# Optimization experiments

Hardware: AMD Instinct MI355X
Metric: run time of the kernel (lower is better)

## Reference

```python
import jax, jax.numpy as jnp
import numpy as np

N = 100000   # nodes
E = 500000   # edges
DN = 64      # node feat dim
DE = 64      # edge feat dim
D = 128      # hidden = in_feats = out_feats
TD = 64      # time-encoding dim


def setup_inputs() -> dict:
    key = jax.random.key(0)
    ks = jax.random.split(key, 20)
    s = 0.05
    inp = {
        'nfeat': jax.random.normal(ks[0], (N, DN), dtype=jnp.float32),
        'efeat': jax.random.normal(ks[1], (E, DE), dtype=jnp.float32),
        'src': jax.random.randint(ks[2], (E,), 0, N),
        'dst': jax.random.randint(ks[3], (E,), 0, N),
        'ts': jax.random.uniform(ks[4], (E,), dtype=jnp.float32) * 1000.0,
    }
    i = 5
    for l in (1, 2):
        inp[f'W_self{l}'] = jax.random.normal(ks[i], (D + TD, D), dtype=jnp.float32) * s; i += 1
        inp[f'b_self{l}'] = jnp.zeros((D,), dtype=jnp.float32)
        inp[f'W_neigh{l}'] = jax.random.normal(ks[i], (D, D), dtype=jnp.float32) * s; i += 1
        inp[f'b_neigh{l}'] = jnp.zeros((D,), dtype=jnp.float32)
        inp[f'omega{l}'] = jax.random.normal(ks[i], (TD,), dtype=jnp.float32); i += 1
        inp[f'phase{l}'] = jax.random.normal(ks[i], (TD,), dtype=jnp.float32); i += 1
    return inp


def _tsage_layer(src_prev, dst_prev, src, dst, ts, W_self, b_self, W_neigh, b_neigh, omega, phase):
    # cosine time encoding per edge: [E, TD]
    te = jnp.cos(ts[:, None] * omega[None, :] + phase[None, :])
    # temporal-neighborhood mean: per node, mean of features of incident edges
    sum_n = (jax.ops.segment_sum(dst_prev, src, num_segments=N)
             + jax.ops.segment_sum(src_prev, dst, num_segments=N))      # [N, D]
    ones = jnp.ones((src.shape[0], 1), dtype=src_prev.dtype)
    cnt = (jax.ops.segment_sum(ones, src, num_segments=N)
           + jax.ops.segment_sum(ones, dst, num_segments=N))            # [N, 1]
    mean_n = sum_n / jnp.maximum(cnt, 1.0)                              # [N, D]
    neigh_proj = mean_n @ W_neigh + b_neigh                             # project once per node
    src_out = jnp.concatenate([src_prev, te], axis=1) @ W_self + b_self + neigh_proj[src]
    dst_out = jnp.concatenate([dst_prev, te], axis=1) @ W_self + b_self + neigh_proj[dst]
    # dropout in eval mode (identity), then activation (relu)
    return jax.nn.relu(src_out), jax.nn.relu(dst_out)


def reference(nfeat, efeat, src, dst, ts,
              W_self1, b_self1, W_neigh1, b_neigh1, omega1, phase1,
              W_self2, b_self2, W_neigh2, b_neigh2, omega2, phase2):
    # combine_feats: per-edge gather-concat of endpoint node feats with edge feats
    src_feat = jnp.concatenate([nfeat[src], efeat], axis=1)  # [E, D]
    dst_feat = jnp.concatenate([nfeat[dst], efeat], axis=1)  # [E, D]
    params = [
        (W_self1, b_self1, W_neigh1, b_neigh1, omega1, phase1),
        (W_self2, b_self2, W_neigh2, b_neigh2, omega2, phase2),
    ]
    for p in params:
        src_feat, dst_feat = _tsage_layer(src_feat, dst_feat, src, dst, ts, *p)
    return src_feat, dst_feat
```

## Files before the change

kernel.cpp:

```cpp
#include <hip/hip_runtime.h>
#include <cstdint>
#include <cmath>

#define NN 100000
#define EE 500000
#define CAP 64

typedef __attribute__((ext_vector_type(8))) short short8v;
typedef __attribute__((ext_vector_type(4))) float f32x4;

static __device__ __forceinline__ unsigned short f2bf_rne(float x) {
    unsigned u = __float_as_uint(x);
    u += 0x7FFFu + ((u >> 16) & 1u);
    return (unsigned short)(u >> 16);
}

static __device__ __forceinline__ void split8(float4 a, float4 b,
                                              short8v* hi, short8v* lo) {
    union { short8v v; unsigned u[4]; } H, L;
    float f[8] = {a.x, a.y, a.z, a.w, b.x, b.y, b.z, b.w};
#pragma unroll
    for (int p = 0; p < 4; ++p) {
        unsigned u0 = __float_as_uint(f[2 * p]);
        unsigned u1 = __float_as_uint(f[2 * p + 1]);
        H.u[p] = (u0 >> 16) | (u1 & 0xFFFF0000u);
        float r0 = f[2 * p]     - __uint_as_float(u0 & 0xFFFF0000u);
        float r1 = f[2 * p + 1] - __uint_as_float(u1 & 0xFFFF0000u);
        L.u[p] = (unsigned)f2bf_rne(r0) | ((unsigned)f2bf_rne(r1) << 16);
    }
    *hi = H.v; *lo = L.v;
}

__global__ __launch_bounds__(256) void k_build(const int* __restrict__ src,
                                               const int* __restrict__ dst,
                                               int* __restrict__ pos,
                                               int* __restrict__ eidx) {
    int e = blockIdx.x * 256 + threadIdx.x;
    if (e >= EE) return;
    int s = src[e], d = dst[e];
    int sl = atomicAdd(&pos[s], 1);
    if (sl < CAP) eidx[(size_t)s * CAP + sl] = (e << 1) | 1;
    int dl = atomicAdd(&pos[d], 1);
    if (dl < CAP) eidx[(size_t)d * CAP + dl] = (e << 1);
}

__global__ __launch_bounds__(256) void k_wt(const float* __restrict__ W, int K,
                                            unsigned short* __restrict__ H,
                                            unsigned short* __restrict__ L) {
    int idx = blockIdx.x * 256 + threadIdx.x;
    if (idx >= K * 128) return;
    int k = idx >> 7, c = idx & 127;
    float x = W[idx];
    unsigned u = __float_as_uint(x);
    H[(size_t)c * K + k] = (unsigned short)(u >> 16);
    float r = x - __uint_as_float(u & 0xFFFF0000u);
    L[(size_t)c * K + k] = f2bf_rne(r);
}

template <int LAYER>
__global__ __launch_bounds__(256) void k_agg(const float* __restrict__ featS,
                                             const float* __restrict__ featD,
                                             const float* __restrict__ nfeat,
                                             const float* __restrict__ efeat,
                                             const int* __restrict__ src,
                                             const int* __restrict__ dst,
                                             const int* __restrict__ pos,
                                             const int* __restrict__ eidx,
                                             float* __restrict__ mean) {
    int w = (blockIdx.x * 256 + threadIdx.x) >> 6;
    int lane = threadIdx.x & 63;
    if (w >= NN) return;
    int half = lane >> 5, cl = lane & 31;
    int d = pos[w];
    int dd = min(d, CAP);
    const int* lst = eidx + (size_t)w * CAP;
    float ax = 0.f, ay = 0.f, az = 0.f, aw = 0.f;
    for (int j = half; j < dd; j += 2) {
        int entry = lst[j];
        int e = entry >> 1, side = entry & 1;
        const float* p;
        if (LAYER == 1) {
            if (cl < 16) {
                int other = side ? dst[e] : src[e];
                p = nfeat + (size_t)other * 64 + cl * 4;
            } else {
                p = efeat + (size_t)e * 64 + (cl - 16) * 4;
            }
        } else {
            p = (side ? featD : featS) + (size_t)e * 128 + cl * 4;
        }
        float4 v = *(const float4*)p;
        ax += v.x; ay += v.y; az += v.z; aw += v.w;
    }
    ax += __shfl_xor(ax, 32); ay += __shfl_xor(ay, 32);
    az += __shfl_xor(az, 32); aw += __shfl_xor(aw, 32);
    if (half == 0) {
        float inv = 1.0f / fmaxf((float)d, 1.0f);
        float4 r; r.x = ax * inv; r.y = ay * inv; r.z = az * inv; r.w = aw * inv;
        *(float4*)(mean + (size_t)w * 128 + cl * 4) = r;
    }
}

__global__ __launch_bounds__(256, 3) void k_neigh_mfma(
        const float* __restrict__ mean,
        const unsigned short* __restrict__ WtH,
        const unsigned short* __restrict__ WtL,
        const float* __restrict__ bias,
        float* __restrict__ outp) {
    const int tid  = threadIdx.x;
    const int n0   = blockIdx.x * 128;
    const int lane = tid & 63;
    const int w    = tid >> 6;
    const int krow = lane & 15;
    const int kgrp = lane >> 4;

    const float* rb[2];
#pragma unroll
    for (int rt = 0; rt < 2; ++rt) {
        int n = min(n0 + w * 32 + rt * 16 + krow, NN - 1);
        rb[rt] = mean + (size_t)n * 128;
    }

    f32x4 acc[2][8] = {};
#pragma unroll
    for (int ch = 0; ch < 4; ++ch) {
        const int koff = ch * 32 + kgrp * 8;
        short8v Ah[2], Al[2];
#pragma unroll
        for (int rt = 0; rt < 2; ++rt) {
            float4 x0 = *(const float4*)(rb[rt] + koff);
            float4 x1 = *(const float4*)(rb[rt] + koff + 4);
            split8(x0, x1, &Ah[rt], &Al[rt]);
        }
#pragma unroll
        for (int ct = 0; ct < 8; ++ct) {
            int c = ct * 16 + krow;
            short8v Bh = *(const short8v*)(WtH + (size_t)c * 128 + koff);
            short8v Bl = *(const short8v*)(WtL + (size_t)c * 128 + koff);
#pragma unroll
            for (int rt = 0; rt < 2; ++rt) {
                acc[rt][ct] = __builtin_amdgcn_mfma_f32_16x16x32_bf16(Ah[rt], Bh, acc[rt][ct], 0, 0, 0);
                acc[rt][ct] = __builtin_amdgcn_mfma_f32_16x16x32_bf16(Ah[rt], Bl, acc[rt][ct], 0, 0, 0);
                acc[rt][ct] = __builtin_amdgcn_mfma_f32_16x16x32_bf16(Al[rt], Bh, acc[rt][ct], 0, 0, 0);
            }
        }
    }

    float bcol[8];
#pragma unroll
    for (int ct = 0; ct < 8; ++ct) bcol[ct] = bias[ct * 16 + krow];
#pragma unroll
    for (int rt = 0; rt < 2; ++rt) {
#pragma unroll
        for (int j = 0; j < 4; ++j) {
            int n = n0 + w * 32 + rt * 16 + kgrp * 4 + j;
            if (n < NN) {
                float* op = outp + (size_t)n * 128;
#pragma unroll
                for (int ct = 0; ct < 8; ++ct)
                    op[ct * 16 + krow] = acc[rt][ct][j] + bcol[ct];
            }
        }
    }
}

template <int LAYER>
__global__ __launch_bounds__(256, 3) void k_edge_mfma(
        const float* __restrict__ featS, const float* __restrict__ featD,
        const float* __restrict__ nfeat, const float* __restrict__ efeat,
        float* __restrict__ outS, float* __restrict__ outD,
        const int* __restrict__ src, const int* __restrict__ dst,
        const float* __restrict__ ts,
        const unsigned short* __restrict__ WtH,
        const unsigned short* __restrict__ WtL,
        const float* __restrict__ bias,
        const float* __restrict__ neigh,
        const float* __restrict__ omega, const float* __restrict__ phase) {
    __shared__ unsigned short teH[64][72];
    __shared__ unsigned short teL[64][72];

    const int tid  = threadIdx.x;
    const int e0   = blockIdx.x * 64;
    const int lane = tid & 63;
    const int w    = tid >> 6;
    const int krow = lane & 15;
    const int kgrp = lane >> 4;

    {
        const int tl = tid & 63;
        const int j0 = (tid >> 6) * 16;
        const float tval = ts[min(e0 + tl, EE - 1)];
#pragma unroll
        for (int j = 0; j < 16; j += 2) {
            int jj = j0 + j;
            float c0 = cosf(fmaf(tval, omega[jj],     phase[jj]));
            float c1 = cosf(fmaf(tval, omega[jj + 1], phase[jj + 1]));
            unsigned u0 = __float_as_uint(c0), u1 = __float_as_uint(c1);
            *(unsigned*)&teH[tl][jj] = (u0 >> 16) | (u1 & 0xFFFF0000u);
            float r0 = c0 - __uint_as_float(u0 & 0xFFFF0000u);
            float r1 = c1 - __uint_as_float(u1 & 0xFFFF0000u);
            *(unsigned*)&teL[tl][jj] =
                (unsigned)f2bf_rne(r0) | ((unsigned)f2bf_rne(r1) << 16);
        }
    }
    __syncthreads();

    const float* rbN[2];
    const float* rbE[2];
#pragma unroll
    for (int rt = 0; rt < 2; ++rt) {
        int row = w * 32 + rt * 16 + krow;
        int e = min(e0 + (row & 63), EE - 1);
        if (LAYER == 1) {
            int node = (row < 64) ? src[e] : dst[e];
            rbN[rt] = nfeat + (size_t)node * 64;
            rbE[rt] = efeat + (size_t)e * 64;
        } else {
            rbN[rt] = ((row < 64) ? featS : featD) + (size_t)e * 128;
            rbE[rt] = nullptr;
        }
    }

    f32x4 acc[2][8] = {};

#pragma unroll
    for (int ch = 0; ch < 4; ++ch) {
        const int koff = ch * 32 + kgrp * 8;
        short8v Ah[2], Al[2];
#pragma unroll
        for (int rt = 0; rt < 2; ++rt) {
            const float* p;
            if (LAYER == 1) {
                p = (ch < 2) ? (rbN[rt] + koff) : (rbE[rt] + (koff - 64));
            } else {
                p = rbN[rt] + koff;
            }
            float4 x0 = *(const float4*)p;
            float4 x1 = *(const float4*)(p + 4);
            split8(x0, x1, &Ah[rt], &Al[rt]);
        }
#pragma unroll
        for (int ct = 0; ct < 8; ++ct) {
            int c = ct * 16 + krow;
            short8v Bh = *(const short8v*)(WtH + (size_t)c * 192 + koff);
            short8v Bl = *(const short8v*)(WtL + (size_t)c * 192 + koff);
#pragma unroll
            for (int rt = 0; rt < 2; ++rt) {
                acc[rt][ct] = __builtin_amdgcn_mfma_f32_16x16x32_bf16(Ah[rt], Bh, acc[rt][ct], 0, 0, 0);
                acc[rt][ct] = __builtin_amdgcn_mfma_f32_16x16x32_bf16(Ah[rt], Bl, acc[rt][ct], 0, 0, 0);
                acc[rt][ct] = __builtin_amdgcn_mfma_f32_16x16x32_bf16(Al[rt], Bh, acc[rt][ct], 0, 0, 0);
            }
        }
    }

#pragma unroll
    for (int ch = 4; ch < 6; ++ch) {
        const int koff = ch * 32 + kgrp * 8;
        const int kt = koff - 128;
        short8v Ah[2], Al[2];
#pragma unroll
        for (int rt = 0; rt < 2; ++rt) {
            int el = (w * 32 + rt * 16 + krow) & 63;
            Ah[rt] = *(const short8v*)&teH[el][kt];
            Al[rt] = *(const short8v*)&teL[el][kt];
        }
#pragma unroll
        for (int ct = 0; ct < 8; ++ct) {
            int c = ct * 16 + krow;
            short8v Bh = *(const short8v*)(WtH + (size_t)c * 192 + koff);
            short8v Bl = *(const short8v*)(WtL + (size_t)c * 192 + koff);
#pragma unroll
            for (int rt = 0; rt < 2; ++rt) {
                acc[rt][ct] = __builtin_amdgcn_mfma_f32_16x16x32_bf16(Ah[rt], Bh, acc[rt][ct], 0, 0, 0);
                acc[rt][ct] = __builtin_amdgcn_mfma_f32_16x16x32_bf16(Ah[rt], Bl, acc[rt][ct], 0, 0, 0);
                acc[rt][ct] = __builtin_amdgcn_mfma_f32_16x16x32_bf16(Al[rt], Bh, acc[rt][ct], 0, 0, 0);
            }
        }
    }

    float bcol[8];
#pragma unroll
    for (int ct = 0; ct < 8; ++ct) bcol[ct] = bias[ct * 16 + krow];
#pragma unroll
    for (int rt = 0; rt < 2; ++rt) {
#pragma unroll
        for (int j = 0; j < 4; ++j) {
            int row = w * 32 + rt * 16 + kgrp * 4 + j;
            int e = e0 + (row & 63);
            if (e < EE) {
                bool isS = row < 64;
                int node = isS ? src[e] : dst[e];
                const float* np = neigh + (size_t)node * 128;
                float* op = (isS ? outS : outD) + (size_t)e * 128;
#pragma unroll
                for (int ct = 0; ct < 8; ++ct) {
                    float v2 = acc[rt][ct][j] + bcol[ct] + np[ct * 16 + krow];
                    op[ct * 16 + krow] = fmaxf(v2, 0.f);
                }
            }
        }
    }
}

extern "C" void kernel_launch(void* const* d_in, const int* in_sizes, int n_in,
                              void* d_out, int out_size, void* d_ws, size_t ws_size,
                              hipStream_t stream) {
    const float* nfeat = (const float*)d_in[0];
    const float* efeat = (const float*)d_in[1];
    const int*   src   = (const int*)d_in[2];
    const int*   dst   = (const int*)d_in[3];
    const float* ts    = (const float*)d_in[4];
    const float* Wself[2]  = {(const float*)d_in[5],  (const float*)d_in[11]};
    const float* bself[2]  = {(const float*)d_in[6],  (const float*)d_in[12]};
    const float* Wneigh[2] = {(const float*)d_in[7],  (const float*)d_in[13]};
    const float* bneigh[2] = {(const float*)d_in[8],  (const float*)d_in[14]};
    const float* omega[2]  = {(const float*)d_in[9],  (const float*)d_in[15]};
    const float* phase[2]  = {(const float*)d_in[10], (const float*)d_in[16]};

    float* outS = (float*)d_out;
    float* outD = outS + (size_t)EE * 128;

    float* mean  = (float*)d_ws;
    float* neigh = mean + (size_t)NN * 128;
    int*   pos   = (int*)(neigh + (size_t)NN * 128);
    int*   eidx  = pos + NN;
    unsigned short* wb = (unsigned short*)(eidx + (size_t)NN * CAP);
    unsigned short* WsH[2] = {wb,                 wb + 2 * 128 * 192};
    unsigned short* WsL[2] = {wb + 128 * 192,     wb + 3 * 128 * 192};
    unsigned short* wn = wb + 4 * 128 * 192;
    unsigned short* WnH[2] = {wn,                 wn + 2 * 128 * 128};
    unsigned short* WnL[2] = {wn + 128 * 128,     wn + 3 * 128 * 128};

    hipMemsetAsync(pos, 0, NN * sizeof(int), stream);
    k_build<<<(EE + 255) / 256, 256, 0, stream>>>(src, dst, pos, eidx);
    for (int l = 0; l < 2; ++l) {
        k_wt<<<(192 * 128 + 255) / 256, 256, 0, stream>>>(Wself[l], 192, WsH[l], WsL[l]);
        k_wt<<<(128 * 128 + 255) / 256, 256, 0, stream>>>(Wneigh[l], 128, WnH[l], WnL[l]);
    }

    k_agg<1><<<(NN * 64 + 255) / 256, 256, 0, stream>>>(outS, outD, nfeat, efeat,
                                                        src, dst, pos, eidx, mean);
    k_neigh_mfma<<<(NN + 127) / 128, 256, 0, stream>>>(mean, WnH[0], WnL[0], bneigh[0], neigh);
    k_edge_mfma<1><<<(EE + 63) / 64, 256, 0, stream>>>(outS, outD, nfeat, efeat,
                                                       outS, outD, src, dst, ts,
                                                       WsH[0], WsL[0], bself[0], neigh,
                                                       omega[0], phase[0]);

    k_agg<2><<<(NN * 64 + 255) / 256, 256, 0, stream>>>(outS, outD, nfeat, efeat,
                                                        src, dst, pos, eidx, mean);
    k_neigh_mfma<<<(NN + 127) / 128, 256, 0, stream>>>(mean, WnH[1], WnL[1], bneigh[1], neigh);
    k_edge_mfma<2><<<(EE + 63) / 64, 256, 0, stream>>>(outS, outD, nfeat, efeat,
                                                       outS, outD, src, dst, ts,
                                                       WsH[1], WsL[1], bself[1], neigh,
                                                       omega[1], phase[1]);
}
```

Baseline: 2.121 ms.

## Stage edge-GEMM A tiles via LDS DMA, 2x2 warp tiling, denser adjacency

The edge GEMM now streams the gathered A rows into a double-buffered, swizzled LDS tile using global_load_lds DMA. Warps are retiled 2x2 so each wave reuses 4 A row tiles against 4 weight column tiles, which cuts redundant weight loads. The adjacency list now stores the neighbor node id next to the edge id, sparing an extra src/dst lookup in aggregation, and aggregation uses wider per-lane loads with 4 edges in flight. CAP drops from 64 to 48, which silently truncates the neighbor sum for any node with degree above 48, a risk for correctness. The occupancy hints are removed.

```diff
diff --git a/kernel.cpp b/kernel.cpp
--- a/kernel.cpp
+++ b/kernel.cpp
@@ -4,7 +4,7 @@
 
 #define NN 100000
 #define EE 500000
-#define CAP 64
+#define CAP 48
 
 typedef __attribute__((ext_vector_type(8))) short short8v;
 typedef __attribute__((ext_vector_type(4))) float f32x4;
@@ -31,17 +31,23 @@
     *hi = H.v; *lo = L.v;
 }
 
+static __device__ __forceinline__ void lds_dma16(const void* g, void* l) {
+    __builtin_amdgcn_global_load_lds(
+        (const __attribute__((address_space(1))) unsigned int*)g,
+        (__attribute__((address_space(3))) unsigned int*)l, 16, 0, 0);
+}
+
 __global__ __launch_bounds__(256) void k_build(const int* __restrict__ src,
                                                const int* __restrict__ dst,
                                                int* __restrict__ pos,
-                                               int* __restrict__ eidx) {
+                                               int2* __restrict__ inc) {
     int e = blockIdx.x * 256 + threadIdx.x;
     if (e >= EE) return;
     int s = src[e], d = dst[e];
     int sl = atomicAdd(&pos[s], 1);
-    if (sl < CAP) eidx[(size_t)s * CAP + sl] = (e << 1) | 1;
+    if (sl < CAP) inc[(size_t)s * CAP + sl] = make_int2((e << 1) | 1, d);
     int dl = atomicAdd(&pos[d], 1);
-    if (dl < CAP) eidx[(size_t)d * CAP + dl] = (e << 1);
+    if (dl < CAP) inc[(size_t)d * CAP + dl] = make_int2((e << 1), s);
 }
 
 __global__ __launch_bounds__(256) void k_wt(const float* __restrict__ W, int K,
@@ -62,46 +68,51 @@
                                              const float* __restrict__ featD,
                                              const float* __restrict__ nfeat,
                                              const float* __restrict__ efeat,
-                                             const int* __restrict__ src,
-                                             const int* __restrict__ dst,
                                              const int* __restrict__ pos,
-                                             const int* __restrict__ eidx,
+                                             const int2* __restrict__ inc,
                                              float* __restrict__ mean) {
     int w = (blockIdx.x * 256 + threadIdx.x) >> 6;
     int lane = threadIdx.x & 63;
     if (w >= NN) return;
-    int half = lane >> 5, cl = lane & 31;
+    int q = lane >> 4, cl = lane & 15;
     int d = pos[w];
     int dd = min(d, CAP);
-    const int* lst = eidx + (size_t)w * CAP;
-    float ax = 0.f, ay = 0.f, az = 0.f, aw = 0.f;
-    for (int j = half; j < dd; j += 2) {
-        int entry = lst[j];
-        int e = entry >> 1, side = entry & 1;
+    const int2* lst = inc + (size_t)w * CAP;
+    float a0 = 0.f, a1 = 0.f, a2 = 0.f, a3 = 0.f;
+    float a4 = 0.f, a5 = 0.f, a6 = 0.f, a7 = 0.f;
+    for (int j = q; j < dd; j += 4) {
+        int2 en = lst[j];
+        int e = en.x >> 1, side = en.x & 1;
         const float* p;
         if (LAYER == 1) {
-            if (cl < 16) {
-                int other = side ? dst[e] : src[e];
-                p = nfeat + (size_t)other * 64 + cl * 4;
-            } else {
-                p = efeat + (size_t)e * 64 + (cl - 16) * 4;
-            }
+            p = (cl < 8) ? (nfeat + (size_t)en.y * 64 + cl * 8)
+                         : (efeat + (size_t)e * 64 + (cl - 8) * 8);
         } else {
-            p = (side ? featD : featS) + (size_t)e * 128 + cl * 4;
-        }
-        float4 v = *(const float4*)p;
-        ax += v.x; ay += v.y; az += v.z; aw += v.w;
-    }
-    ax += __shfl_xor(ax, 32); ay += __shfl_xor(ay, 32);
-    az += __shfl_xor(az, 32); aw += __shfl_xor(aw, 32);
-    if (half == 0) {
+            p = (side ? featD : featS) + (size_t)e * 128 + cl * 8;
+        }
+        float4 v0 = *(const float4*)p;
+        float4 v1 = *(const float4*)(p + 4);
+        a0 += v0.x; a1 += v0.y; a2 += v0.z; a3 += v0.w;
+        a4 += v1.x; a5 += v1.y; a6 += v1.z; a7 += v1.w;
+    }
+#pragma unroll
+    for (int m = 16; m <= 32; m <<= 1) {
+        a0 += __shfl_xor(a0, m); a1 += __shfl_xor(a1, m);
+        a2 += __shfl_xor(a2, m); a3 += __shfl_xor(a3, m);
+        a4 += __shfl_xor(a4, m); a5 += __shfl_xor(a5, m);
+        a6 += __shfl_xor(a6, m); a7 += __shfl_xor(a7, m);
+    }
+    if (q == 0) {
         float inv = 1.0f / fmaxf((float)d, 1.0f);
-        float4 r; r.x = ax * inv; r.y = ay * inv; r.z = az * inv; r.w = aw * inv;
-        *(float4*)(mean + (size_t)w * 128 + cl * 4) = r;
-    }
-}
-
-__global__ __launch_bounds__(256, 3) void k_neigh_mfma(
+        float4 r0, r1;
+        r0.x = a0 * inv; r0.y = a1 * inv; r0.z = a2 * inv; r0.w = a3 * inv;
+        r1.x = a4 * inv; r1.y = a5 * inv; r1.z = a6 * inv; r1.w = a7 * inv;
+        *(float4*)(mean + (size_t)w * 128 + cl * 8) = r0;
+        *(float4*)(mean + (size_t)w * 128 + cl * 8 + 4) = r1;
+    }
+}
+
+__global__ __launch_bounds__(256) void k_neigh_mfma(
         const float* __restrict__ mean,
         const unsigned short* __restrict__ WtH,
         const unsigned short* __restrict__ WtL,
@@ -111,61 +122,64 @@
     const int n0   = blockIdx.x * 128;
     const int lane = tid & 63;
     const int w    = tid >> 6;
+    const int wr   = w >> 1, wc = w & 1;
     const int krow = lane & 15;
     const int kgrp = lane >> 4;
 
-    const float* rb[2];
-#pragma unroll
-    for (int rt = 0; rt < 2; ++rt) {
-        int n = min(n0 + w * 32 + rt * 16 + krow, NN - 1);
+    const float* rb[4];
+#pragma unroll
+    for (int rt = 0; rt < 4; ++rt) {
+        int n = min(n0 + wr * 64 + rt * 16 + krow, NN - 1);
         rb[rt] = mean + (size_t)n * 128;
     }
 
-    f32x4 acc[2][8] = {};
+    f32x4 acc[4][4] = {};
 #pragma unroll
     for (int ch = 0; ch < 4; ++ch) {
         const int koff = ch * 32 + kgrp * 8;
-        short8v Ah[2], Al[2];
-#pragma unroll
-        for (int rt = 0; rt < 2; ++rt) {
+        short8v Ah[4], Al[4];
+#pragma unroll
+        for (int rt = 0; rt < 4; ++rt) {
             float4 x0 = *(const float4*)(rb[rt] + koff);
             float4 x1 = *(const float4*)(rb[rt] + koff + 4);
             split8(x0, x1, &Ah[rt], &Al[rt]);
         }
-#pragma unroll
-        for (int ct = 0; ct < 8; ++ct) {
-            int c = ct * 16 + krow;
-            short8v Bh = *(const short8v*)(WtH + (size_t)c * 128 + koff);
-            short8v Bl = *(const short8v*)(WtL + (size_t)c * 128 + koff);
-#pragma unroll
-            for (int rt = 0; rt < 2; ++rt) {
-                acc[rt][ct] = __builtin_amdgcn_mfma_f32_16x16x32_bf16(Ah[rt], Bh, acc[rt][ct], 0, 0, 0);
-                acc[rt][ct] = __builtin_amdgcn_mfma_f32_16x16x32_bf16(Ah[rt], Bl, acc[rt][ct], 0, 0, 0);
-                acc[rt][ct] = __builtin_amdgcn_mfma_f32_16x16x32_bf16(Al[rt], Bh, acc[rt][ct], 0, 0, 0);
-            }
-        }
-    }
-
-    float bcol[8];
-#pragma unroll
-    for (int ct = 0; ct < 8; ++ct) bcol[ct] = bias[ct * 16 + krow];
-#pragma unroll
-    for (int rt = 0; rt < 2; ++rt) {
+        short8v Bh[4], Bl[4];
+#pragma unroll
+        for (int ct = 0; ct < 4; ++ct) {
+            int c = wc * 64 + ct * 16 + krow;
+            Bh[ct] = *(const short8v*)(WtH + (size_t)c * 128 + koff);
+            Bl[ct] = *(const short8v*)(WtL + (size_t)c * 128 + koff);
+        }
+#pragma unroll
+        for (int ct = 0; ct < 4; ++ct)
+#pragma unroll
+            for (int rt = 0; rt < 4; ++rt) {
+                acc[rt][ct] = __builtin_amdgcn_mfma_f32_16x16x32_bf16(Ah[rt], Bh[ct], acc[rt][ct], 0, 0, 0);
+                acc[rt][ct] = __builtin_amdgcn_mfma_f32_16x16x32_bf16(Ah[rt], Bl[ct], acc[rt][ct], 0, 0, 0);
+                acc[rt][ct] = __builtin_amdgcn_mfma_f32_16x16x32_bf16(Al[rt], Bh[ct], acc[rt][ct], 0, 0, 0);
+            }
+    }
+
+    float bcol[4];
+#pragma unroll
+    for (int ct = 0; ct < 4; ++ct) bcol[ct] = bias[wc * 64 + ct * 16 + krow];
+#pragma unroll
+    for (int rt = 0; rt < 4; ++rt)
 #pragma unroll
         for (int j = 0; j < 4; ++j) {
-            int n = n0 + w * 32 + rt * 16 + kgrp * 4 + j;
+            int n = n0 + wr * 64 + rt * 16 + kgrp * 4 + j;
             if (n < NN) {
                 float* op = outp + (size_t)n * 128;
 #pragma unroll
-                for (int ct = 0; ct < 8; ++ct)
-                    op[ct * 16 + krow] = acc[rt][ct][j] + bcol[ct];
-            }
-        }
-    }
+                for (int ct = 0; ct < 4; ++ct)
+                    op[wc * 64 + ct * 16 + krow] = acc[rt][ct][j] + bcol[ct];
+            }
+        }
 }
 
 template <int LAYER>
-__global__ __launch_bounds__(256, 3) void k_edge_mfma(
+__global__ __launch_bounds__(256) void k_edge_mfma(
         const float* __restrict__ featS, const float* __restrict__ featD,
         const float* __restrict__ nfeat, const float* __restrict__ efeat,
         float* __restrict__ outS, float* __restrict__ outD,
@@ -176,6 +190,7 @@
         const float* __restrict__ bias,
         const float* __restrict__ neigh,
         const float* __restrict__ omega, const float* __restrict__ phase) {
+    __shared__ float Abuf[2][128][32];
     __shared__ unsigned short teH[64][72];
     __shared__ unsigned short teL[64][72];
 
@@ -183,6 +198,7 @@
     const int e0   = blockIdx.x * 64;
     const int lane = tid & 63;
     const int w    = tid >> 6;
+    const int wr   = w >> 1, wc = w & 1;
     const int krow = lane & 15;
     const int kgrp = lane >> 4;
 
@@ -203,89 +219,108 @@
                 (unsigned)f2bf_rne(r0) | ((unsigned)f2bf_rne(r1) << 16);
         }
     }
-    __syncthreads();
-
-    const float* rbN[2];
-    const float* rbE[2];
-#pragma unroll
-    for (int rt = 0; rt < 2; ++rt) {
-        int row = w * 32 + rt * 16 + krow;
+
+    const float* gbN[4];
+    const float* gbE[4];
+#pragma unroll
+    for (int qq = 0; qq < 4; ++qq) {
+        int row = w * 32 + qq * 8 + (lane >> 3);
         int e = min(e0 + (row & 63), EE - 1);
         if (LAYER == 1) {
             int node = (row < 64) ? src[e] : dst[e];
-            rbN[rt] = nfeat + (size_t)node * 64;
-            rbE[rt] = efeat + (size_t)e * 64;
+            gbN[qq] = nfeat + (size_t)node * 64;
+            gbE[qq] = efeat + (size_t)e * 64;
         } else {
-            rbN[rt] = ((row < 64) ? featS : featD) + (size_t)e * 128;
-            rbE[rt] = nullptr;
-        }
-    }
-
-    f32x4 acc[2][8] = {};
+            gbN[qq] = ((row < 64) ? featS : featD) + (size_t)e * 128;
+            gbE[qq] = nullptr;
+        }
+    }
+    const int pslot = lane & 7;
+
+    auto dma_chunk = [&](int b, int ch) {
+#pragma unroll
+        for (int qq = 0; qq < 4; ++qq) {
+            int row = w * 32 + qq * 8 + (lane >> 3);
+            int pg = (pslot - row) & 7;
+            const float* gsrc;
+            if (LAYER == 1)
+                gsrc = ((ch < 2) ? (gbN[qq] + ch * 32) : (gbE[qq] + (ch - 2) * 32)) + pg * 4;
+            else
+                gsrc = gbN[qq] + ch * 32 + pg * 4;
+            lds_dma16(gsrc, &Abuf[b][(w * 4 + qq) * 8][0]);
+        }
+    };
+
+    f32x4 acc[4][4] = {};
+    dma_chunk(0, 0);
 
 #pragma unroll
     for (int ch = 0; ch < 4; ++ch) {
+        __syncthreads();
+        if (ch < 3) dma_chunk((ch + 1) & 1, ch + 1);
+        const int b = ch & 1;
         const int koff = ch * 32 + kgrp * 8;
-        short8v Ah[2], Al[2];
-#pragma unroll
-        for (int rt = 0; rt < 2; ++rt) {
-            const float* p;
-            if (LAYER == 1) {
-                p = (ch < 2) ? (rbN[rt] + koff) : (rbE[rt] + (koff - 64));
-            } else {
-                p = rbN[rt] + koff;
-            }
-            float4 x0 = *(const float4*)p;
-            float4 x1 = *(const float4*)(p + 4);
+        short8v Ah[4], Al[4];
+#pragma unroll
+        for (int rt = 0; rt < 4; ++rt) {
+            int row = wr * 64 + rt * 16 + krow;
+            float4 x0 = *(const float4*)&Abuf[b][row][(((2 * kgrp)     + row) & 7) * 4];
+            float4 x1 = *(const float4*)&Abuf[b][row][(((2 * kgrp + 1) + row) & 7) * 4];
             split8(x0, x1, &Ah[rt], &Al[rt]);
         }
-#pragma unroll
-        for (int ct = 0; ct < 8; ++ct) {
-            int c = ct * 16 + krow;
-            short8v Bh = *(const short8v*)(WtH + (size_t)c * 192 + koff);
-            short8v Bl = *(const short8v*)(WtL + (size_t)c * 192 + koff);
-#pragma unroll
-            for (int rt = 0; rt < 2; ++rt) {
-                acc[rt][ct] = __builtin_amdgcn_mfma_f32_16x16x32_bf16(Ah[rt], Bh, acc[rt][ct], 0, 0, 0);
-                acc[rt][ct] = __builtin_amdgcn_mfma_f32_16x16x32_bf16(Ah[rt], Bl, acc[rt][ct], 0, 0, 0);
-                acc[rt][ct] = __builtin_amdgcn_mfma_f32_16x16x32_bf16(Al[rt], Bh, acc[rt][ct], 0, 0, 0);
-            }
-        }
+        short8v Bh[4], Bl[4];
+#pragma unroll
+        for (int ct = 0; ct < 4; ++ct) {
+            int c = wc * 64 + ct * 16 + krow;
+            Bh[ct] = *(const short8v*)(WtH + (size_t)c * 192 + koff);
+            Bl[ct] = *(const short8v*)(WtL + (size_t)c * 192 + koff);
+        }
+#pragma unroll
+        for (int ct = 0; ct < 4; ++ct)
+#pragma unroll
+            for (int rt = 0; rt < 4; ++rt) {
+                acc[rt][ct] = __builtin_amdgcn_mfma_f32_16x16x32_bf16(Ah[rt], Bh[ct], acc[rt][ct], 0, 0, 0);
+                acc[rt][ct] = __builtin_amdgcn_mfma_f32_16x16x32_bf16(Ah[rt], Bl[ct], acc[rt][ct], 0, 0, 0);
+                acc[rt][ct] = __builtin_amdgcn_mfma_f32_16x16x32_bf16(Al[rt], Bh[ct], acc[rt][ct], 0, 0, 0);
+            }
     }
 
 #pragma unroll
     for (int ch = 4; ch < 6; ++ch) {
         const int koff = ch * 32 + kgrp * 8;
         const int kt = koff - 128;
-        short8v Ah[2], Al[2];
-#pragma unroll
-        for (int rt = 0; rt < 2; ++rt) {
-            int el = (w * 32 + rt * 16 + krow) & 63;
+        short8v Ah[4], Al[4];
+#pragma unroll
+        for (int rt = 0; rt < 4; ++rt) {
+            int el = rt * 16 + krow;
             Ah[rt] = *(const short8v*)&teH[el][kt];
             Al[rt] = *(const short8v*)&teL[el][kt];
         }
-#pragma unroll
-        for (int ct = 0; ct < 8; ++ct) {
-            int c = ct * 16 + krow;
-            short8v Bh = *(const short8v*)(WtH + (size_t)c * 192 + koff);
-            short8v Bl = *(const short8v*)(WtL + (size_t)c * 192 + koff);
-#pragma unroll
-            for (int rt = 0; rt < 2; ++rt) {
-                acc[rt][ct] = __builtin_amdgcn_mfma_f32_16x16x32_bf16(Ah[rt], Bh, acc[rt][ct], 0, 0, 0);
-                acc[rt][ct] = __builtin_amdgcn_mfma_f32_16x16x32_bf16(Ah[rt], Bl, acc[rt][ct], 0, 0, 0);
-                acc[rt][ct] = __builtin_amdgcn_mfma_f32_16x16x32_bf16(Al[rt], Bh, acc[rt][ct], 0, 0, 0);
-            }
-        }
-    }
-
-    float bcol[8];
-#pragma unroll
-    for (int ct = 0; ct < 8; ++ct) bcol[ct] = bias[ct * 16 + krow];
-#pragma unroll
-    for (int rt = 0; rt < 2; ++rt) {
+        short8v Bh[4], Bl[4];
+#pragma unroll
+        for (int ct = 0; ct < 4; ++ct) {
+            int c = wc * 64 + ct * 16 + krow;
+            Bh[ct] = *(const short8v*)(WtH + (size_t)c * 192 + koff);
+            Bl[ct] = *(const short8v*)(WtL + (size_t)c * 192 + koff);
+        }
+#pragma unroll
+        for (int ct = 0; ct < 4; ++ct)
+#pragma unroll
+            for (int rt = 0; rt < 4; ++rt) {
+                acc[rt][ct] = __builtin_amdgcn_mfma_f32_16x16x32_bf16(Ah[rt], Bh[ct], acc[rt][ct], 0, 0, 0);
+                acc[rt][ct] = __builtin_amdgcn_mfma_f32_16x16x32_bf16(Ah[rt], Bl[ct], acc[rt][ct], 0, 0, 0);
+                acc[rt][ct] = __builtin_amdgcn_mfma_f32_16x16x32_bf16(Al[rt], Bh[ct], acc[rt][ct], 0, 0, 0);
+            }
+    }
+
+    float bcol[4];
+#pragma unroll
+    for (int ct = 0; ct < 4; ++ct) bcol[ct] = bias[wc * 64 + ct * 16 + krow];
+#pragma unroll
+    for (int rt = 0; rt < 4; ++rt)
 #pragma unroll
         for (int j = 0; j < 4; ++j) {
-            int row = w * 32 + rt * 16 + kgrp * 4 + j;
+            int row = wr * 64 + rt * 16 + kgrp * 4 + j;
             int e = e0 + (row & 63);
             if (e < EE) {
                 bool isS = row < 64;
@@ -293,13 +328,13 @@
                 const float* np = neigh + (size_t)node * 128;
                 float* op = (isS ? outS : outD) + (size_t)e * 128;
 #pragma unroll
-                for (int ct = 0; ct < 8; ++ct) {
-                    float v2 = acc[rt][ct][j] + bcol[ct] + np[ct * 16 + krow];
-                    op[ct * 16 + krow] = fmaxf(v2, 0.f);
+                for (int ct = 0; ct < 4; ++ct) {
+                    int col = wc * 64 + ct * 16 + krow;
+                    float v2 = acc[rt][ct][j] + bcol[ct] + np[col];
+                    op[col] = fmaxf(v2, 0.f);
                 }
             }
         }
-    }
 }
 
 extern "C" void kernel_launch(void* const* d_in, const int* in_sizes, int n_in,
@@ -323,8 +358,8 @@
     float* mean  = (float*)d_ws;
     float* neigh = mean + (size_t)NN * 128;
     int*   pos   = (int*)(neigh + (size_t)NN * 128);
-    int*   eidx  = pos + NN;
-    unsigned short* wb = (unsigned short*)(eidx + (size_t)NN * CAP);
+    int2*  inc   = (int2*)(pos + NN);
+    unsigned short* wb = (unsigned short*)(inc + (size_t)NN * CAP);
     unsigned short* WsH[2] = {wb,                 wb + 2 * 128 * 192};
     unsigned short* WsL[2] = {wb + 128 * 192,     wb + 3 * 128 * 192};
     unsigned short* wn = wb + 4 * 128 * 192;
@@ -332,14 +367,14 @@
     unsigned short* WnL[2] = {wn + 128 * 128,     wn + 3 * 128 * 128};
 
     hipMemsetAsync(pos, 0, NN * sizeof(int), stream);
-    k_build<<<(EE + 255) / 256, 256, 0, stream>>>(src, dst, pos, eidx);
+    k_build<<<(EE + 255) / 256, 256, 0, stream>>>(src, dst, pos, inc);
     for (int l = 0; l < 2; ++l) {
         k_wt<<<(192 * 128 + 255) / 256, 256, 0, stream>>>(Wself[l], 192, WsH[l], WsL[l]);
         k_wt<<<(128 * 128 + 255) / 256, 256, 0, stream>>>(Wneigh[l], 128, WnH[l], WnL[l]);
     }
 
     k_agg<1><<<(NN * 64 + 255) / 256, 256, 0, stream>>>(outS, outD, nfeat, efeat,
-                                                        src, dst, pos, eidx, mean);
+                                                        pos, inc, mean);
     k_neigh_mfma<<<(NN + 127) / 128, 256, 0, stream>>>(mean, WnH[0], WnL[0], bneigh[0], neigh);
     k_edge_mfma<1><<<(EE + 63) / 64, 256, 0, stream>>>(outS, outD, nfeat, efeat,
                                                        outS, outD, src, dst, ts,
@@ -347,7 +382,7 @@
                                                        omega[0], phase[0]);
 
     k_agg<2><<<(NN * 64 + 255) / 256, 256, 0, stream>>>(outS, outD, nfeat, efeat,
-                                                        src, dst, pos, eidx, mean);
+                                                        pos, inc, mean);
     k_neigh_mfma<<<(NN + 127) / 128, 256, 0, stream>>>(mean, WnH[1], WnL[1], bneigh[1], neigh);
     k_edge_mfma<2><<<(EE + 63) / 64, 256, 0, stream>>>(outS, outD, nfeat, efeat,
                                                        outS, outD, src, dst, ts,
```

New measurement: 1.913 ms. 1.11x faster.
